# Kernel tuning notes

Hardware: AMD Instinct MI355X
Metric: run time of the kernel (lower is better)

## Reference

```python
import jax, jax.numpy as jnp
import numpy as np

B, C_IN, H, W = 4, 16, 64, 64
OUT_C, K, STRIDE = 32, 3, 1
NUM_DEG = 6   # numerator coeffs for x^0..x^5 (order[0]+1)
DEN_DEG = 4


def setup_inputs() -> dict:
    key = jax.random.key(0)
    k1, k2, k3 = jax.random.split(key, 3)
    x = jax.random.normal(k1, (B, C_IN, H, W), dtype=jnp.float32)
    nums = 0.1 * jax.random.normal(k2, (OUT_C * C_IN * K * K, NUM_DEG), dtype=jnp.float32)
    denoms = 0.1 * jax.random.normal(k3, (OUT_C * C_IN * K * K, DEN_DEG), dtype=jnp.float32)
    return {"input": x, "nums": nums, "denoms": denoms}


def _ka_conv(x, nums, denoms):
    pad = (K - 1) // 2
    xp = jnp.pad(x, ((0, 0), (0, 0), (pad, pad), (pad, pad)))
    Ho = (x.shape[2] + 2 * pad - K) // STRIDE + 1
    Wo = (x.shape[3] + 2 * pad - K) // STRIDE + 1
    # patches [B, C, K*K, Ho, Wo] ordered (c, ki, kj) to match nums row layout
    patches = jnp.stack(
        [xp[:, :, i:i + STRIDE * Ho:STRIDE, j:j + STRIDE * Wo:STRIDE]
         for i in range(K) for j in range(K)], axis=2)
    M = C_IN * K * K
    patches = patches.reshape(x.shape[0], M, Ho, Wo)
    # powers x^0..x^5 built by cumulative products (grad-safe at x=0)
    pows = [jnp.ones_like(patches)]
    for _ in range(NUM_DEG - 1):
        pows.append(pows[-1] * patches)
    pw = jnp.stack(pows, axis=-1)  # [B, M, Ho, Wo, NUM_DEG]
    a = nums.reshape(OUT_C, M, NUM_DEG)
    b = denoms.reshape(OUT_C, M, DEN_DEG)
    # per-weight rational: P/Q for every (out_channel, weight, position)
    num = jnp.einsum('bmhwp,omp->bomhw', pw, a)
    den = 1.0 + jnp.abs(jnp.einsum('bmhwq,omq->bomhw', pw[..., 1:1 + DEN_DEG], b))
    return jnp.sum(num / den, axis=2)  # [B, OUT_C, Ho, Wo]


def reference(input, nums, denoms):
    return _ka_conv(input, nums, denoms)
```

## Files before the change

### kernel.cpp

```cpp
#include <hip/hip_runtime.h>
#include <hip/hip_fp16.h>


constexpr int Bn = 4, Cin = 16, Hh = 64, Ww = 64, Oc = 32, Mtot = 144;
constexpr int PW = 66;
constexpr size_t WSX_FLOATS = (size_t)Bn * Cin * PW * PW;
constexpr int NREC = Oc * Mtot;

__global__ __launch_bounds__(256)
void ka_prep_kernel(const float* __restrict__ x,
                    const float* __restrict__ nums,
                    const float* __restrict__ denoms,
                    float* __restrict__ wsf) {
  const int blk = blockIdx.x;
  if (blk < Bn * Cin) {
    const float* __restrict__ xp = x + (size_t)blk * Hh * Ww;
    float* __restrict__ wp_ = wsf + (size_t)blk * PW * PW;
    for (int i = threadIdx.x; i < PW * PW; i += 256) {
      const int hp = i / PW, wq = i % PW;
      const bool in = (hp >= 1) & (hp <= Hh) & (wq >= 1) & (wq <= Ww);
      wp_[i] = in ? xp[(hp - 1) * Ww + (wq - 1)] : 0.f;
    }
  } else {
    const int idx = (blk - Bn * Cin) * 256 + threadIdx.x;
    if (idx < NREC) {
      const float* __restrict__ a = nums + (size_t)idx * 6;
      const float* __restrict__ c = denoms + (size_t)idx * 4;
      unsigned int* __restrict__ r =
          (unsigned int*)(wsf + WSX_FLOATS) + (size_t)idx * 12;
      #pragma unroll
      for (int k = 0; k < 6; ++k) {
        const unsigned short h = __half_as_ushort(__float2half_rn(a[k]));
        r[k] = ((unsigned int)h << 16) | h;
      }
      #pragma unroll
      for (int k = 0; k < 4; ++k) {
        const unsigned short h = __half_as_ushort(__float2half_rn(c[k]));
        r[6 + k] = ((unsigned int)h << 16) | h;
      }
      r[10] = 0u; r[11] = 0u;
    }
  }
}

__device__ __forceinline__ __half2 u2h2(unsigned int u) {
  union { unsigned int u; __half2 h; } cv;
  cv.u = u;
  return cv.h;
}

__global__ __launch_bounds__(256, 4)
void ka_conv_kernel(const float* __restrict__ wsf, float* __restrict__ out) {
  const int tid = threadIdx.x;
  const int n   = blockIdx.x;
  const int ht  = n & 7;
  const int o   = __builtin_amdgcn_readfirstlane((n >> 3) & 31);
  const int b   = n >> 8;

  const int w  = tid & 63;
  const int rg = tid >> 6;
  const int h0 = ht * 8 + rg * 2;

  const float* __restrict__ xb = wsf + (size_t)b * Cin * PW * PW;
  const unsigned int* __restrict__ coef =
      (const unsigned int*)(wsf + WSX_FLOATS) + (size_t)o * Mtot * 12;

  __half2 acc0 = __floats2half2_rn(0.f, 0.f);
  __half2 acc1 = acc0, acc2 = acc0;
  const __half2 one2 = __floats2half2_rn(1.f, 1.f);

#define TAP(t, vp, accK) do {                                                  \
    const unsigned int* __restrict__ rr = pc + (t) * 12;                       \
    const __half2 v_ = (vp);                                                   \
    __half2 nm = __hfma2(u2h2(rr[5]), v_, u2h2(rr[4]));                        \
    nm = __hfma2(nm, v_, u2h2(rr[3]));                                         \
    nm = __hfma2(nm, v_, u2h2(rr[2]));                                         \
    nm = __hfma2(nm, v_, u2h2(rr[1]));                                         \
    nm = __hfma2(nm, v_, u2h2(rr[0]));                                         \
    __half2 dp = __hfma2(u2h2(rr[9]), v_, u2h2(rr[8]));                        \
    dp = __hfma2(dp, v_, u2h2(rr[7]));                                         \
    dp = __hfma2(dp, v_, u2h2(rr[6]));                                         \
    dp = __hmul2(dp, v_);                                                      \
    const __half2 dn = __hadd2(one2, __habs2(dp));                             \
    accK = __hfma2(nm, h2rcp(dn), accK);                                       \
  } while (0)

  #pragma unroll 2
  for (int c = 0; c < Cin; ++c) {
    const float* __restrict__ xc = xb + (size_t)c * (PW * PW);
    const float* __restrict__ p0 = xc + (h0 + 0) * PW + w;
    const float* __restrict__ p1 = xc + (h0 + 1) * PW + w;
    const float* __restrict__ p2 = xc + (h0 + 2) * PW + w;
    const float* __restrict__ p3 = xc + (h0 + 3) * PW + w;

    const float x00 = p0[0], x01 = p0[1], x02 = p0[2];
    const float x10 = p1[0], x11 = p1[1], x12 = p1[2];
    const float x20 = p2[0], x21 = p2[1], x22 = p2[2];
    const float x30 = p3[0], x31 = p3[1], x32 = p3[2];

    const __half2 q00 = __floats2half2_rn(x00, x10);
    const __half2 q01 = __floats2half2_rn(x01, x11);
    const __half2 q02 = __floats2half2_rn(x02, x12);
    const __half2 q10 = __floats2half2_rn(x10, x20);
    const __half2 q11 = __floats2half2_rn(x11, x21);
    const __half2 q12 = __floats2half2_rn(x12, x22);
    const __half2 q20 = __floats2half2_rn(x20, x30);
    const __half2 q21 = __floats2half2_rn(x21, x31);
    const __half2 q22 = __floats2half2_rn(x22, x32);

    const unsigned int* __restrict__ pc = coef + (size_t)c * 9 * 12;
    TAP(0, q00, acc0);  TAP(1, q01, acc1);  TAP(2, q02, acc2);
    TAP(3, q10, acc0);  TAP(4, q11, acc1);  TAP(5, q12, acc2);
    TAP(6, q20, acc0);  TAP(7, q21, acc1);  TAP(8, q22, acc2);
  }
#undef TAP

  const float2 f0 = __half22float2(acc0);
  const float2 f1 = __half22float2(acc1);
  const float2 f2 = __half22float2(acc2);
  float* op = out + ((size_t)(b * Oc + o) * Hh + h0) * Ww + w;
  op[0]  = f0.x + f1.x + f2.x;
  op[Ww] = f0.y + f1.y + f2.y;
}

extern "C" void kernel_launch(void* const* d_in, const int* in_sizes, int n_in,
                              void* d_out, int out_size, void* d_ws, size_t ws_size,
                              hipStream_t stream) {
  const float* x      = (const float*)d_in[0];
  const float* nums   = (const float*)d_in[1];
  const float* denoms = (const float*)d_in[2];
  float* out          = (float*)d_out;
  float* ws           = (float*)d_ws;

  const int padBlocks = Bn * Cin;
  const int recBlocks = (NREC + 255) / 256;
  ka_prep_kernel<<<padBlocks + recBlocks, 256, 0, stream>>>(x, nums, denoms, ws);

  ka_conv_kernel<<<Bn * Oc * 8, 256, 0, stream>>>(ws, out);
}
```

Before: 34.23 us.

## Split input channels across waves with shared-memory reduction, four rows per thread

The conv kernel now gives each of the four waves in a block a quarter of the input channels. Each thread computes four output rows (two half2 pairs) and reuses each coefficient load across both pairs. Partial sums are combined through LDS after a barrier, and the grid doubles so more blocks cover the output. This raises parallelism and coefficient reuse per load. The cost is an LDS reduction and a __syncthreads per block, plus higher register pressure from six accumulators.

Result: slower. 45.86 us (+34.0%).

```diff
diff --git a/kernel.cpp b/kernel.cpp
--- a/kernel.cpp
+++ b/kernel.cpp
@@ -44,83 +44,106 @@
 }
 
 __device__ __forceinline__ __half2 u2h2(unsigned int u) {
-  union { unsigned int u; __half2 h; } cv;
-  cv.u = u;
-  return cv.h;
+  union { unsigned int u; __half2 h; } cv; cv.u = u; return cv.h;
 }
 
 __global__ __launch_bounds__(256, 4)
 void ka_conv_kernel(const float* __restrict__ wsf, float* __restrict__ out) {
+  __shared__ float part[1024];
+
   const int tid = threadIdx.x;
   const int n   = blockIdx.x;
-  const int ht  = n & 7;
-  const int o   = __builtin_amdgcn_readfirstlane((n >> 3) & 31);
-  const int b   = n >> 8;
+  const int ht  = n & 15;
+  const int o   = __builtin_amdgcn_readfirstlane((n >> 4) & 31);
+  const int b   = n >> 9;
 
   const int w  = tid & 63;
-  const int rg = tid >> 6;
-  const int h0 = ht * 8 + rg * 2;
+  const int q  = tid >> 6;
+  const int h0 = ht * 4;
 
   const float* __restrict__ xb = wsf + (size_t)b * Cin * PW * PW;
   const unsigned int* __restrict__ coef =
       (const unsigned int*)(wsf + WSX_FLOATS) + (size_t)o * Mtot * 12;
 
-  __half2 acc0 = __floats2half2_rn(0.f, 0.f);
-  __half2 acc1 = acc0, acc2 = acc0;
+  __half2 a0A = __floats2half2_rn(0.f, 0.f);
+  __half2 a1A = a0A, a2A = a0A, a0B = a0A, a1B = a0A, a2B = a0A;
   const __half2 one2 = __floats2half2_rn(1.f, 1.f);
 
-#define TAP(t, vp, accK) do {                                                  \
+#define TAP4(t, vA, vB, accA, accB) do {                                       \
     const unsigned int* __restrict__ rr = pc + (t) * 12;                       \
-    const __half2 v_ = (vp);                                                   \
-    __half2 nm = __hfma2(u2h2(rr[5]), v_, u2h2(rr[4]));                        \
-    nm = __hfma2(nm, v_, u2h2(rr[3]));                                         \
-    nm = __hfma2(nm, v_, u2h2(rr[2]));                                         \
-    nm = __hfma2(nm, v_, u2h2(rr[1]));                                         \
-    nm = __hfma2(nm, v_, u2h2(rr[0]));                                         \
-    __half2 dp = __hfma2(u2h2(rr[9]), v_, u2h2(rr[8]));                        \
-    dp = __hfma2(dp, v_, u2h2(rr[7]));                                         \
-    dp = __hfma2(dp, v_, u2h2(rr[6]));                                         \
-    dp = __hmul2(dp, v_);                                                      \
-    const __half2 dn = __hadd2(one2, __habs2(dp));                             \
-    accK = __hfma2(nm, h2rcp(dn), accK);                                       \
+    __half2 nA = __hfma2(u2h2(rr[5]), (vA), u2h2(rr[4]));                      \
+    __half2 nB = __hfma2(u2h2(rr[5]), (vB), u2h2(rr[4]));                      \
+    nA = __hfma2(nA, (vA), u2h2(rr[3]));  nB = __hfma2(nB, (vB), u2h2(rr[3])); \
+    nA = __hfma2(nA, (vA), u2h2(rr[2]));  nB = __hfma2(nB, (vB), u2h2(rr[2])); \
+    nA = __hfma2(nA, (vA), u2h2(rr[1]));  nB = __hfma2(nB, (vB), u2h2(rr[1])); \
+    nA = __hfma2(nA, (vA), u2h2(rr[0]));  nB = __hfma2(nB, (vB), u2h2(rr[0])); \
+    __half2 dA = __hfma2(u2h2(rr[9]), (vA), u2h2(rr[8]));                      \
+    __half2 dB = __hfma2(u2h2(rr[9]), (vB), u2h2(rr[8]));                      \
+    dA = __hfma2(dA, (vA), u2h2(rr[7]));  dB = __hfma2(dB, (vB), u2h2(rr[7])); \
+    dA = __hfma2(dA, (vA), u2h2(rr[6]));  dB = __hfma2(dB, (vB), u2h2(rr[6])); \
+    dA = __hmul2(dA, (vA));               dB = __hmul2(dB, (vB));              \
+    const __half2 eA = __hadd2(one2, __habs2(dA));                             \
+    const __half2 eB = __hadd2(one2, __habs2(dB));                             \
+    accA = __hfma2(nA, h2rcp(eA), accA);                                       \
+    accB = __hfma2(nB, h2rcp(eB), accB);                                       \
   } while (0)
 
   #pragma unroll 2
-  for (int c = 0; c < Cin; ++c) {
+  for (int ci = 0; ci < 4; ++ci) {
+    const int c = q * 4 + ci;
     const float* __restrict__ xc = xb + (size_t)c * (PW * PW);
-    const float* __restrict__ p0 = xc + (h0 + 0) * PW + w;
-    const float* __restrict__ p1 = xc + (h0 + 1) * PW + w;
-    const float* __restrict__ p2 = xc + (h0 + 2) * PW + w;
-    const float* __restrict__ p3 = xc + (h0 + 3) * PW + w;
+    const int base = h0 * PW + w;
 
-    const float x00 = p0[0], x01 = p0[1], x02 = p0[2];
-    const float x10 = p1[0], x11 = p1[1], x12 = p1[2];
-    const float x20 = p2[0], x21 = p2[1], x22 = p2[2];
-    const float x30 = p3[0], x31 = p3[1], x32 = p3[2];
+    float x0j0 = xc[base + 0 * PW + 0], x0j1 = xc[base + 0 * PW + 1], x0j2 = xc[base + 0 * PW + 2];
+    float x1j0 = xc[base + 1 * PW + 0], x1j1 = xc[base + 1 * PW + 1], x1j2 = xc[base + 1 * PW + 2];
+    float x2j0 = xc[base + 2 * PW + 0], x2j1 = xc[base + 2 * PW + 1], x2j2 = xc[base + 2 * PW + 2];
+    float x3j0 = xc[base + 3 * PW + 0], x3j1 = xc[base + 3 * PW + 1], x3j2 = xc[base + 3 * PW + 2];
+    float x4j0 = xc[base + 4 * PW + 0], x4j1 = xc[base + 4 * PW + 1], x4j2 = xc[base + 4 * PW + 2];
+    float x5j0 = xc[base + 5 * PW + 0], x5j1 = xc[base + 5 * PW + 1], x5j2 = xc[base + 5 * PW + 2];
 
-    const __half2 q00 = __floats2half2_rn(x00, x10);
-    const __half2 q01 = __floats2half2_rn(x01, x11);
-    const __half2 q02 = __floats2half2_rn(x02, x12);
-    const __half2 q10 = __floats2half2_rn(x10, x20);
-    const __half2 q11 = __floats2half2_rn(x11, x21);
-    const __half2 q12 = __floats2half2_rn(x12, x22);
-    const __half2 q20 = __floats2half2_rn(x20, x30);
-    const __half2 q21 = __floats2half2_rn(x21, x31);
-    const __half2 q22 = __floats2half2_rn(x22, x32);
+    const __half2 h01j0 = __floats2half2_rn(x0j0, x1j0);
+    const __half2 h01j1 = __floats2half2_rn(x0j1, x1j1);
+    const __half2 h01j2 = __floats2half2_rn(x0j2, x1j2);
+    const __half2 h12j0 = __floats2half2_rn(x1j0, x2j0);
+    const __half2 h12j1 = __floats2half2_rn(x1j1, x2j1);
+    const __half2 h12j2 = __floats2half2_rn(x1j2, x2j2);
+    const __half2 h23j0 = __floats2half2_rn(x2j0, x3j0);
+    const __half2 h23j1 = __floats2half2_rn(x2j1, x3j1);
+    const __half2 h23j2 = __floats2half2_rn(x2j2, x3j2);
+    const __half2 h34j0 = __floats2half2_rn(x3j0, x4j0);
+    const __half2 h34j1 = __floats2half2_rn(x3j1, x4j1);
+    const __half2 h34j2 = __floats2half2_rn(x3j2, x4j2);
+    const __half2 h45j0 = __floats2half2_rn(x4j0, x5j0);
+    const __half2 h45j1 = __floats2half2_rn(x4j1, x5j1);
+    const __half2 h45j2 = __floats2half2_rn(x4j2, x5j2);
 
     const unsigned int* __restrict__ pc = coef + (size_t)c * 9 * 12;
-    TAP(0, q00, acc0);  TAP(1, q01, acc1);  TAP(2, q02, acc2);
-    TAP(3, q10, acc0);  TAP(4, q11, acc1);  TAP(5, q12, acc2);
-    TAP(6, q20, acc0);  TAP(7, q21, acc1);  TAP(8, q22, acc2);
+    TAP4(0, h01j0, h23j0, a0A, a0B);
+    TAP4(1, h01j1, h23j1, a1A, a1B);
+    TAP4(2, h01j2, h23j2, a2A, a2B);
+    TAP4(3, h12j0, h34j0, a0A, a0B);
+    TAP4(4, h12j1, h34j1, a1A, a1B);
+    TAP4(5, h12j2, h34j2, a2A, a2B);
+    TAP4(6, h23j0, h45j0, a0A, a0B);
+    TAP4(7, h23j1, h45j1, a1A, a1B);
+    TAP4(8, h23j2, h45j2, a2A, a2B);
   }
-#undef TAP
+#undef TAP4
 
-  const float2 f0 = __half22float2(acc0);
-  const float2 f1 = __half22float2(acc1);
-  const float2 f2 = __half22float2(acc2);
-  float* op = out + ((size_t)(b * Oc + o) * Hh + h0) * Ww + w;
-  op[0]  = f0.x + f1.x + f2.x;
-  op[Ww] = f0.y + f1.y + f2.y;
+  const float2 fA = __half22float2(__hadd2(__hadd2(a0A, a1A), a2A));
+  const float2 fB = __half22float2(__hadd2(__hadd2(a0B, a1B), a2B));
+  part[q * 256 +   0 + w] = fA.x;
+  part[q * 256 +  64 + w] = fA.y;
+  part[q * 256 + 128 + w] = fB.x;
+  part[q * 256 + 192 + w] = fB.y;
+  __syncthreads();
+
+  if (tid < 256) {
+    const int row = tid >> 6, ww = tid & 63;
+    const int s = row * 64 + ww;
+    const float v = ((part[s] + part[256 + s]) + part[512 + s]) + part[768 + s];
+    out[((size_t)(b * Oc + o) * Hh + h0 + row) * Ww + ww] = v;
+  }
 }
 
 extern "C" void kernel_launch(void* const* d_in, const int* in_sizes, int n_in,
@@ -136,5 +159,5 @@
   const int recBlocks = (NREC + 255) / 256;
   ka_prep_kernel<<<padBlocks + recBlocks, 256, 0, stream>>>(x, nums, denoms, ws);
 
-  ka_conv_kernel<<<Bn * Oc * 8, 256, 0, stream>>>(ws, out);
+  ka_conv_kernel<<<Bn * Oc * 16, 256, 0, stream>>>(ws, out);
 }
```
